# Performance work log

Measured on AMD Instinct MI355X. Metric: run time of the kernel, lower is better.

The kernel has to match this reference:

```python
import jax, jax.numpy as jnp
import numpy as np

D_MODEL = 768
N_HEAD = 12


def setup_inputs() -> dict:
    key = jax.random.key(0)
    ks = jax.random.split(key, 5)
    B, S, D = 2, 4096, D_MODEL
    scale = 0.02
    return {
        "x": jax.random.normal(ks[0], (B, S, D), dtype=jnp.float32),
        "W_in": jax.random.normal(ks[1], (D, 3 * D), dtype=jnp.float32) * scale,
        "b_in": jax.random.normal(ks[2], (3 * D,), dtype=jnp.float32) * scale,
        "W_out": jax.random.normal(ks[3], (D, D), dtype=jnp.float32) * scale,
        "b_out": jax.random.normal(ks[4], (D,), dtype=jnp.float32) * scale,
    }


def reference(x, W_in, b_in, W_out, b_out):
    B, S, D = x.shape
    H = N_HEAD
    d_head = D // H
    qkv = x @ W_in + b_in                      # [B,S,3D]
    q, k, v = jnp.split(qkv, 3, axis=-1)
    # [B,H,S,d]
    q = q.reshape(B, S, H, d_head).transpose(0, 2, 1, 3)
    k = k.reshape(B, S, H, d_head).transpose(0, 2, 1, 3)
    v = v.reshape(B, S, H, d_head).transpose(0, 2, 1, 3)
    att = jnp.einsum("bhqd,bhkd->bhqk", q, k) * (1.0 / jnp.sqrt(jnp.float32(d_head)))
    causal = jnp.tril(jnp.ones((S, S), dtype=bool))
    att = jnp.where(causal[None, None], att, jnp.float32(-jnp.inf))
    att = jax.nn.softmax(att, axis=-1)
    y = jnp.einsum("bhqk,bhkd->bhqd", att, v)  # [B,H,S,d]
    y = y.transpose(0, 2, 1, 3).reshape(B, S, D)
    return y @ W_out + b_out
```

## Files before the change

### kernel.cpp

```cpp
#include <hip/hip_runtime.h>
#include <hip/hip_bf16.h>


#define D_MODEL 768
#define SEQ 4096
#define NB 2
#define NHEAD 12

typedef __attribute__((ext_vector_type(8))) short short8;
typedef __attribute__((ext_vector_type(4))) float floatx4;
typedef __attribute__((ext_vector_type(16))) float floatx16;

#define SM_C 0.18033688011112042f

#if __has_builtin(__builtin_amdgcn_exp2f)
#define EXP2(x) __builtin_amdgcn_exp2f(x)
#else
#define EXP2(x) __expf((x) * 0.6931471805599453f)
#endif

__device__ inline short fb(float f) {
    union { __hip_bfloat16 h; short s; } cv;
    cv.h = __float2bfloat16(f);
    return cv.s;
}
__device__ inline unsigned pk2(float a, float b) {
    float2 f; f.x = a; f.y = b;
    union { __hip_bfloat162 h; unsigned u; } cv;
    cv.h = __float22bfloat162_rn(f);
    return cv.u;
}
__device__ inline void gload16(const void* g, void* l) {
    __builtin_amdgcn_global_load_lds(
        (const __attribute__((address_space(1))) unsigned int*)g,
        (__attribute__((address_space(3))) unsigned int*)l, 16, 0, 0);
}

__global__ __launch_bounds__(256) void convert_bf16(const float* __restrict__ src,
                                                    short* __restrict__ dst, size_t n) {
    size_t i = ((size_t)blockIdx.x * 256 + threadIdx.x) * 8;
    if (i >= n) return;
    float4 f0 = *(const float4*)(src + i);
    float4 f1 = *(const float4*)(src + i + 4);
    uint4 u = {pk2(f0.x, f0.y), pk2(f0.z, f0.w), pk2(f1.x, f1.y), pk2(f1.z, f1.w)};
    *(uint4*)(dst + i) = u;
}

__global__ __launch_bounds__(256) void transpose_bf16(const float* __restrict__ W,
                                                      short* __restrict__ Wt,
                                                      int K, int N) {
    __shared__ short t[32][33];
    const int n0 = blockIdx.x * 32, k0 = blockIdx.y * 32;
    const int tx = threadIdx.x, ty = threadIdx.y;
#pragma unroll
    for (int j = 0; j < 4; ++j)
        t[ty + j * 8][tx] = fb(W[(size_t)(k0 + ty + j * 8) * N + n0 + tx]);
    __syncthreads();
#pragma unroll
    for (int j = 0; j < 4; ++j)
        Wt[(size_t)(n0 + ty + j * 8) * K + k0 + tx] = t[tx][ty + j * 8];
}

__global__ __launch_bounds__(256) void gemm_qkv128(const short* __restrict__ A,
                                                   const short* __restrict__ Bt,
                                                   const float* __restrict__ bias,
                                                   short* __restrict__ qimg,
                                                   short* __restrict__ kimg,
                                                   short* __restrict__ vimg) {
    const int K = D_MODEL;
    __shared__ short As[128][32];
    __shared__ short Bs[128][32];
    const int tid = threadIdx.x, lane = tid & 63, w = tid >> 6;
    const int wr = w >> 1, wc = w & 1;
    const int lo = lane & 15, hi = lane >> 4;
    const int m0 = blockIdx.y * 128, n0 = blockIdx.x * 128;
    const int lr = lane >> 2, lc = (lane & 3) * 8;

    floatx4 acc[4][4] = {};
    const short* Ag = A  + (size_t)(m0 + w * 16 + lr) * K + lc;
    const short* Bg = Bt + (size_t)(n0 + w * 16 + lr) * K + lc;

    for (int k0 = 0; k0 < K; k0 += 32) {
        __syncthreads();
        gload16(Ag + k0,                  &As[w * 16][0]);
        gload16(Ag + k0 + (size_t)64 * K, &As[64 + w * 16][0]);
        gload16(Bg + k0,                  &Bs[w * 16][0]);
        gload16(Bg + k0 + (size_t)64 * K, &Bs[64 + w * 16][0]);
        __syncthreads();
        short8 a[4], bf[4];
#pragma unroll
        for (int m = 0; m < 4; ++m) a[m] = *(const short8*)&As[wr * 64 + m * 16 + lo][hi * 8];
#pragma unroll
        for (int n = 0; n < 4; ++n) bf[n] = *(const short8*)&Bs[wc * 64 + n * 16 + lo][hi * 8];
#pragma unroll
        for (int m = 0; m < 4; ++m)
#pragma unroll
            for (int n = 0; n < 4; ++n)
                acc[m][n] = __builtin_amdgcn_mfma_f32_16x16x32_bf16(a[m], bf[n], acc[m][n], 0, 0, 0);
    }

#pragma unroll
    for (int m = 0; m < 4; ++m)
#pragma unroll
        for (int n = 0; n < 4; ++n) {
            int col  = n0 + wc * 64 + n * 16 + lo;
            int row0 = m0 + wr * 64 + m * 16 + hi * 4;
            float bv = bias[col];
            if (col < D_MODEL) {
                int hq = col >> 6, dh = col & 63;
                int kc = dh >> 4, dl = (dh >> 3) & 1, d7 = dh & 7;
#pragma unroll
                for (int r = 0; r < 4; ++r) {
                    int row = row0 + r;
                    int bb = row >> 12, s = row & 4095;
                    size_t off = (((((size_t)bb * NHEAD + hq) * 64 + (s >> 6)) * 8
                                  + ((s >> 5) & 1) * 4 + kc) * 512)
                               + ((s & 31) + dl * 32) * 8 + d7;
                    qimg[off] = fb((acc[m][n][r] + bv) * SM_C);
                }
            } else if (col < 2 * D_MODEL) {
                int kc2 = col - D_MODEL;
                int hh = kc2 >> 6, dh = kc2 & 63;
                int kc = dh >> 4, dl = (dh >> 3) & 1, d7 = dh & 7;
#pragma unroll
                for (int r = 0; r < 4; ++r) {
                    int row = row0 + r;
                    int bb = row >> 12, s = row & 4095;
                    int kb = s >> 6, kr = s & 63;
                    size_t base = (((size_t)bb * NHEAD + hh) * 64 + kb) * 4096;
                    kimg[base + ((kr >> 5) * 4 + kc) * 512 + ((kr & 31) + dl * 32) * 8 + d7] =
                        fb(acc[m][n][r] + bv);
                }
            } else {
                int vcol = col - 2 * D_MODEL;
                int hh = vcol >> 6, dh = vcol & 63;
                int bb = row0 >> 12, s = row0 & 4095;
                int kb = s >> 6, kr = s & 63;
                size_t base = (((size_t)bb * NHEAD + hh) * 64 + kb) * 4096;
                size_t off = base + ((dh >> 5) * 4 + (kr >> 4)) * 512
                           + ((dh & 31) + ((kr >> 3) & 1) * 32) * 8 + (kr & 7);
                uint2 u = {pk2(acc[m][n][0] + bv, acc[m][n][1] + bv),
                           pk2(acc[m][n][2] + bv, acc[m][n][3] + bv)};
                *(uint2*)&vimg[off] = u;
            }
        }
}

__global__ __launch_bounds__(256) void gemm_out128(const short* __restrict__ A,
                                                   const short* __restrict__ Bt,
                                                   const float* __restrict__ bias,
                                                   float* __restrict__ C) {
    const int K = D_MODEL, N = D_MODEL;
    __shared__ short As[128][32];
    __shared__ short Bs[128][32];
    const int tid = threadIdx.x, lane = tid & 63, w = tid >> 6;
    const int wr = w >> 1, wc = w & 1;
    const int lo = lane & 15, hi = lane >> 4;
    const int m0 = blockIdx.y * 128, n0 = blockIdx.x * 128;
    const int lr = lane >> 2, lc = (lane & 3) * 8;

    floatx4 acc[4][4] = {};
    const short* Ag = A  + (size_t)(m0 + w * 16 + lr) * K + lc;
    const short* Bg = Bt + (size_t)(n0 + w * 16 + lr) * K + lc;

    for (int k0 = 0; k0 < K; k0 += 32) {
        __syncthreads();
        gload16(Ag + k0,                  &As[w * 16][0]);
        gload16(Ag + k0 + (size_t)64 * K, &As[64 + w * 16][0]);
        gload16(Bg + k0,                  &Bs[w * 16][0]);
        gload16(Bg + k0 + (size_t)64 * K, &Bs[64 + w * 16][0]);
        __syncthreads();
        short8 a[4], bf[4];
#pragma unroll
        for (int m = 0; m < 4; ++m) a[m] = *(const short8*)&As[wr * 64 + m * 16 + lo][hi * 8];
#pragma unroll
        for (int n = 0; n < 4; ++n) bf[n] = *(const short8*)&Bs[wc * 64 + n * 16 + lo][hi * 8];
#pragma unroll
        for (int m = 0; m < 4; ++m)
#pragma unroll
            for (int n = 0; n < 4; ++n)
                acc[m][n] = __builtin_amdgcn_mfma_f32_16x16x32_bf16(a[m], bf[n], acc[m][n], 0, 0, 0);
    }

#pragma unroll
    for (int m = 0; m < 4; ++m)
#pragma unroll
        for (int n = 0; n < 4; ++n) {
            int col  = n0 + wc * 64 + n * 16 + lo;
            int row0 = m0 + wr * 64 + m * 16 + hi * 4;
            float bv = bias[col];
#pragma unroll
            for (int r = 0; r < 4; ++r)
                C[(size_t)(row0 + r) * N + col] = acc[m][n][r] + bv;
        }
}

__global__ __launch_bounds__(256, 2) void attn_k(const short* __restrict__ qimg,
                                                 const short* __restrict__ kimg,
                                                 const short* __restrict__ vimg,
                                                 short* __restrict__ y) {
    const int L = blockIdx.x;
    const int xcd = L & 7, slot = L >> 3;
    const int ghead = slot >> 5, ip = slot & 31;
    const int g = ghead * 8 + xcd;
    const int b = g / NHEAD, h = g % NHEAD;
    const int tid = threadIdx.x, lane = tid & 63, w = tid >> 6;
    const int l31 = lane & 31, hh = lane >> 5;

    __shared__ alignas(16) short KL[4][4096];
    __shared__ unsigned LOD[4][2048];
    __shared__ float LS[4][2][2][64];

    const short* kbase = kimg + ((size_t)b * NHEAD + h) * 64 * 4096;
    const short* vbase = vimg + ((size_t)b * NHEAD + h) * 64 * 4096 + lane * 8;
    const short* qtbase = qimg + ((size_t)b * NHEAD + h) * 64 * 4096;
    short* Kbuf = &KL[w][0];

    const int nlo = ip + 1;
    const int npos = ((64 - w) >> 2) + 1;

    if (w >= nlo) {
#pragma unroll
        for (int r = 0; r < 32; ++r) LOD[w][r * 64 + lane] = 0u;
        LS[w][0][0][lane] = 0.0f;
        LS[w][0][1][lane] = 0.0f;
    }

    floatx16 Oa = {}, Ob = {}, Oc = {}, Od = {};
    float ls0 = 0.0f, ls1 = 0.0f;
    short8 qf0[4], qf1[4], vf[8];

    int curtile = (w < nlo) ? ip : (63 - ip);
    {
        const short* qr = qtbase + (size_t)curtile * 4096 + lane * 8;
#pragma unroll
        for (int kc = 0; kc < 4; ++kc) {
            qf0[kc] = *(const short8*)(qr + kc * 512);
            qf1[kc] = *(const short8*)(qr + (4 + kc) * 512);
        }
    }
    {
        int kb0 = (w < nlo) ? w : (w - nlo);
        const short* ks = kbase + (size_t)kb0 * 4096 + lane * 8;
#pragma unroll
        for (int c = 0; c < 8; ++c) gload16(ks + c * 512, Kbuf + c * 512);
        const short* vs = vbase + (size_t)kb0 * 4096;
#pragma unroll
        for (int i = 0; i < 8; ++i) vf[i] = *(const short8*)(vs + i * 512);
    }

    for (int it = 0; it < npos; ++it) {
        const int s = w + 4 * it;
        const int tile = (s < nlo) ? ip : (63 - ip);
        const int kblk = (s < nlo) ? s : (s - nlo);

        if (tile != curtile) {
#pragma unroll
            for (int rp = 0; rp < 8; ++rp) {
                LOD[w][(0 * 8 + rp) * 64 + lane] = pk2(Oa[2 * rp], Oa[2 * rp + 1]);
                LOD[w][(1 * 8 + rp) * 64 + lane] = pk2(Ob[2 * rp], Ob[2 * rp + 1]);
                LOD[w][(2 * 8 + rp) * 64 + lane] = pk2(Oc[2 * rp], Oc[2 * rp + 1]);
                LOD[w][(3 * 8 + rp) * 64 + lane] = pk2(Od[2 * rp], Od[2 * rp + 1]);
            }
            LS[w][0][0][lane] = ls0;
            LS[w][0][1][lane] = ls1;
#pragma unroll
            for (int r = 0; r < 16; ++r) { Oa[r] = 0.0f; Ob[r] = 0.0f; Oc[r] = 0.0f; Od[r] = 0.0f; }
            ls0 = ls1 = 0.0f;
            const short* qr = qtbase + (size_t)tile * 4096 + lane * 8;
#pragma unroll
            for (int kc = 0; kc < 4; ++kc) {
                qf0[kc] = *(const short8*)(qr + kc * 512);
                qf1[kc] = *(const short8*)(qr + (4 + kc) * 512);
            }
            curtile = tile;
        }

        asm volatile("s_waitcnt vmcnt(0)" ::: "memory");
        __builtin_amdgcn_sched_barrier(0);

        floatx16 S00 = {}, S10 = {}, S01 = {}, S11 = {};
        __builtin_amdgcn_s_setprio(1);
#pragma unroll
        for (int kc = 0; kc < 4; ++kc) {
            short8 kf = *(const short8*)&Kbuf[kc * 512 + lane * 8];
            S00 = __builtin_amdgcn_mfma_f32_32x32x16_bf16(kf, qf0[kc], S00, 0, 0, 0);
            S10 = __builtin_amdgcn_mfma_f32_32x32x16_bf16(kf, qf1[kc], S10, 0, 0, 0);
        }
#pragma unroll
        for (int kc = 0; kc < 4; ++kc) {
            short8 kf = *(const short8*)&Kbuf[(4 + kc) * 512 + lane * 8];
            S01 = __builtin_amdgcn_mfma_f32_32x32x16_bf16(kf, qf0[kc], S01, 0, 0, 0);
            S11 = __builtin_amdgcn_mfma_f32_32x32x16_bf16(kf, qf1[kc], S11, 0, 0, 0);
        }
        __builtin_amdgcn_s_setprio(0);
        __builtin_amdgcn_sched_barrier(0);

        if (it + 1 < npos) {
            int sn = s + 4;
            int nk = (sn < nlo) ? sn : (sn - nlo);
            const short* ks = kbase + (size_t)nk * 4096 + lane * 8;
#pragma unroll
            for (int c = 0; c < 8; ++c) gload16(ks + c * 512, Kbuf + c * 512);
        }
        __builtin_amdgcn_sched_barrier(0);

        if (kblk == tile) {
            const int qg0 = tile * 64 + l31, qg1 = qg0 + 32;
#pragma unroll
            for (int kb2 = 0; kb2 < 2; ++kb2) {
                int kb_base = kblk * 64 + kb2 * 32 + 4 * hh;
#pragma unroll
                for (int r = 0; r < 16; ++r) {
                    int kgl = kb_base + (r & 3) + 8 * (r >> 2);
                    if (kb2 == 0) {
                        if (kgl > qg0) S00[r] = -1e30f;
                        if (kgl > qg1) S10[r] = -1e30f;
                    } else {
                        if (kgl > qg0) S01[r] = -1e30f;
                        if (kgl > qg1) S11[r] = -1e30f;
                    }
                }
            }
        }

#pragma unroll
        for (int kb2 = 0; kb2 < 2; ++kb2) {
            {
                floatx16& S = kb2 ? S01 : S00;
                unsigned wA[4], wB[4];
#pragma unroll
                for (int g4 = 0; g4 < 4; ++g4) {
                    float p0 = EXP2(S[4 * g4 + 0]), p1 = EXP2(S[4 * g4 + 1]);
                    float p2 = EXP2(S[4 * g4 + 2]), p3 = EXP2(S[4 * g4 + 3]);
                    ls0 += (p0 + p1) + (p2 + p3);
                    wA[g4] = pk2(p0, p1);
                    wB[g4] = pk2(p2, p3);
                }
#pragma unroll
                for (int c16 = 0; c16 < 2; ++c16) {
                    unsigned xa = wA[2 * c16], ya = wA[2 * c16 + 1];
                    unsigned xb = wB[2 * c16], yb = wB[2 * c16 + 1];
                    asm("v_permlane32_swap_b32 %0, %1" : "+v"(xa), "+v"(ya));
                    asm("v_permlane32_swap_b32 %0, %1" : "+v"(xb), "+v"(yb));
                    union { unsigned u[4]; short8 s8; } pa;
                    pa.u[0] = xa; pa.u[1] = xb; pa.u[2] = ya; pa.u[3] = yb;
                    const int kcg = kb2 * 2 + c16;
                    __builtin_amdgcn_s_setprio(1);
                    Oa = __builtin_amdgcn_mfma_f32_32x32x16_bf16(pa.s8, vf[kcg],     Oa, 0, 0, 0);
                    Ob = __builtin_amdgcn_mfma_f32_32x32x16_bf16(pa.s8, vf[4 + kcg], Ob, 0, 0, 0);
                    __builtin_amdgcn_s_setprio(0);
                }
            }
            {
                floatx16& S = kb2 ? S11 : S10;
                unsigned wA[4], wB[4];
#pragma unroll
                for (int g4 = 0; g4 < 4; ++g4) {
                    float p0 = EXP2(S[4 * g4 + 0]), p1 = EXP2(S[4 * g4 + 1]);
                    float p2 = EXP2(S[4 * g4 + 2]), p3 = EXP2(S[4 * g4 + 3]);
                    ls1 += (p0 + p1) + (p2 + p3);
                    wA[g4] = pk2(p0, p1);
                    wB[g4] = pk2(p2, p3);
                }
#pragma unroll
                for (int c16 = 0; c16 < 2; ++c16) {
                    unsigned xa = wA[2 * c16], ya = wA[2 * c16 + 1];
                    unsigned xb = wB[2 * c16], yb = wB[2 * c16 + 1];
                    asm("v_permlane32_swap_b32 %0, %1" : "+v"(xa), "+v"(ya));
                    asm("v_permlane32_swap_b32 %0, %1" : "+v"(xb), "+v"(yb));
                    union { unsigned u[4]; short8 s8; } pa;
                    pa.u[0] = xa; pa.u[1] = xb; pa.u[2] = ya; pa.u[3] = yb;
                    const int kcg = kb2 * 2 + c16;
                    __builtin_amdgcn_s_setprio(1);
                    Oc = __builtin_amdgcn_mfma_f32_32x32x16_bf16(pa.s8, vf[kcg],     Oc, 0, 0, 0);
                    Od = __builtin_amdgcn_mfma_f32_32x32x16_bf16(pa.s8, vf[4 + kcg], Od, 0, 0, 0);
                    __builtin_amdgcn_s_setprio(0);
                }
            }
        }
        __builtin_amdgcn_sched_barrier(0);

        if (it + 1 < npos) {
            int sn = s + 4;
            int nk = (sn < nlo) ? sn : (sn - nlo);
            const short* vs = vbase + (size_t)nk * 4096;
#pragma unroll
            for (int i = 0; i < 8; ++i) vf[i] = *(const short8*)(vs + i * 512);
        }
        __builtin_amdgcn_sched_barrier(0);
    }

    {
        unsigned* hslot = (unsigned*)&KL[w][0];
#pragma unroll
        for (int rp = 0; rp < 8; ++rp) {
            hslot[(0 * 8 + rp) * 64 + lane] = pk2(Oa[2 * rp], Oa[2 * rp + 1]);
            hslot[(1 * 8 + rp) * 64 + lane] = pk2(Ob[2 * rp], Ob[2 * rp + 1]);
            hslot[(2 * 8 + rp) * 64 + lane] = pk2(Oc[2 * rp], Oc[2 * rp + 1]);
            hslot[(3 * 8 + rp) * 64 + lane] = pk2(Od[2 * rp], Od[2 * rp + 1]);
        }
        LS[w][1][0][lane] = ls0;
        LS[w][1][1][lane] = ls1;
    }
    __syncthreads();

    {
        const int tsel = w >> 1;
        const int fqh = w & 1;
        const int ftile = tsel ? (63 - ip) : ip;

        float lt = 0.0f;
#pragma unroll
        for (int ww = 0; ww < 4; ++ww)
            lt += LS[ww][tsel][fqh][l31] + LS[ww][tsel][fqh][l31 + 32];
        float inv = 1.0f / lt;

#pragma unroll
        for (int dv = 0; dv < 2; ++dv) {
#pragma unroll
            for (int rp = 0; rp < 8; ++rp) {
                float o0 = 0.0f, o1 = 0.0f;
#pragma unroll
                for (int ww = 0; ww < 4; ++ww) {
                    unsigned u = tsel
                        ? ((const unsigned*)&KL[ww][0])[((fqh * 2 + dv) * 8 + rp) * 64 + lane]
                        : LOD[ww][((fqh * 2 + dv) * 8 + rp) * 64 + lane];
                    o0 += __builtin_bit_cast(float, u << 16);
                    o1 += __builtin_bit_cast(float, u & 0xffff0000u);
                }
                int r0 = 2 * rp, r1 = 2 * rp + 1;
                int q0r = (r0 & 3) + 8 * (r0 >> 2) + 4 * hh;
                int q1r = (r1 & 3) + 8 * (r1 >> 2) + 4 * hh;
                float iv0 = __shfl(inv, q0r, 64);
                float iv1 = __shfl(inv, q1r, 64);
                size_t rowb = ((size_t)b * SEQ + ftile * 64 + fqh * 32);
                y[(rowb + q0r) * D_MODEL + h * 64 + dv * 32 + l31] = fb(o0 * iv0);
                y[(rowb + q1r) * D_MODEL + h * 64 + dv * 32 + l31] = fb(o1 * iv1);
            }
        }
    }
}

extern "C" void kernel_launch(void* const* d_in, const int* in_sizes, int n_in,
                              void* d_out, int out_size, void* d_ws, size_t ws_size,
                              hipStream_t stream) {
    (void)in_sizes; (void)n_in; (void)out_size; (void)ws_size;
    const float* x     = (const float*)d_in[0];
    const float* W_in  = (const float*)d_in[1];
    const float* b_in  = (const float*)d_in[2];
    const float* W_out = (const float*)d_in[3];
    const float* b_out = (const float*)d_in[4];
    float* out = (float*)d_out;

    const int M = NB * SEQ;
    char* p = (char*)d_ws;
    short* xbf   = (short*)p; p += (size_t)M * D_MODEL * 2;
    short* wtin  = (short*)p; p += (size_t)3 * D_MODEL * D_MODEL * 2;
    short* wtout = (short*)p; p += (size_t)D_MODEL * D_MODEL * 2;
    short* qimg  = (short*)p; p += (size_t)M * D_MODEL * 2;
    short* kimg  = (short*)p; p += (size_t)NB * NHEAD * 64 * 4096 * 2;
    short* vimg  = (short*)p; p += (size_t)NB * NHEAD * 64 * 4096 * 2;
    short* yw    = (short*)p;

    convert_bf16<<<dim3((unsigned)((size_t)M * D_MODEL / 8 / 256)), 256, 0, stream>>>(
        x, xbf, (size_t)M * D_MODEL);
    transpose_bf16<<<dim3(3 * D_MODEL / 32, D_MODEL / 32), dim3(32, 8), 0, stream>>>(
        W_in, wtin, D_MODEL, 3 * D_MODEL);
    transpose_bf16<<<dim3(D_MODEL / 32, D_MODEL / 32), dim3(32, 8), 0, stream>>>(
        W_out, wtout, D_MODEL, D_MODEL);
    gemm_qkv128<<<dim3(3 * D_MODEL / 128, M / 128), 256, 0, stream>>>(
        xbf, wtin, b_in, qimg, kimg, vimg);
    attn_k<<<dim3(NB * NHEAD * 32), 256, 0, stream>>>(qimg, kimg, vimg, yw);
    gemm_out128<<<dim3(D_MODEL / 128, M / 128), 256, 0, stream>>>(yw, wtout, b_out, out);
}
```

Baseline: 165.2 us.

## Double-buffer V fragments in registers to prefetch next V block earlier

Splits the V register fragments into two ping-pong buffers and unrolls the loop by two, so the next block's V loads are issued at the start of each iteration instead of after the PV MFMAs. The wait before the QK step becomes vmcnt(8), which waits on the earlier K loads while leaving the fresh V loads in flight. The aim is to hide V global-load latency behind QK and softmax compute. In exchange it uses 32 more VGPRs per lane, which may hurt occupancy at the 2-blocks bound or cause spills, and adds an explicit lgkmcnt wait before the K refill.

```diff
diff --git a/kernel.cpp b/kernel.cpp
--- a/kernel.cpp
+++ b/kernel.cpp
@@ -211,7 +211,7 @@
     __shared__ unsigned LOD[4][2048];
     __shared__ float LS[4][2][2][64];
 
-    const short* kbase = kimg + ((size_t)b * NHEAD + h) * 64 * 4096;
+    const short* kbase = kimg + ((size_t)b * NHEAD + h) * 64 * 4096 + lane * 8;
     const short* vbase = vimg + ((size_t)b * NHEAD + h) * 64 * 4096 + lane * 8;
     const short* qtbase = qimg + ((size_t)b * NHEAD + h) * 64 * 4096;
     short* Kbuf = &KL[w][0];
@@ -228,7 +228,7 @@
 
     floatx16 Oa = {}, Ob = {}, Oc = {}, Od = {};
     float ls0 = 0.0f, ls1 = 0.0f;
-    short8 qf0[4], qf1[4], vf[8];
+    short8 qf0[4], qf1[4], vfA[8], vfB[8];
 
     int curtile = (w < nlo) ? ip : (63 - ip);
     {
@@ -241,15 +241,15 @@
     }
     {
         int kb0 = (w < nlo) ? w : (w - nlo);
-        const short* ks = kbase + (size_t)kb0 * 4096 + lane * 8;
+        const short* ks = kbase + (size_t)kb0 * 4096;
 #pragma unroll
         for (int c = 0; c < 8; ++c) gload16(ks + c * 512, Kbuf + c * 512);
         const short* vs = vbase + (size_t)kb0 * 4096;
 #pragma unroll
-        for (int i = 0; i < 8; ++i) vf[i] = *(const short8*)(vs + i * 512);
-    }
-
-    for (int it = 0; it < npos; ++it) {
+        for (int i = 0; i < 8; ++i) vfA[i] = *(const short8*)(vs + i * 512);
+    }
+
+    auto body = [&](int it, short8 (&vcur)[8], short8 (&vnxt)[8]) {
         const int s = w + 4 * it;
         const int tile = (s < nlo) ? ip : (63 - ip);
         const int kblk = (s < nlo) ? s : (s - nlo);
@@ -276,7 +276,16 @@
             curtile = tile;
         }
 
-        asm volatile("s_waitcnt vmcnt(0)" ::: "memory");
+        const bool more = (it + 1 < npos);
+        if (more) {
+            int sn = s + 4;
+            int nk = (sn < nlo) ? sn : (sn - nlo);
+            const short* vs = vbase + (size_t)nk * 4096;
+#pragma unroll
+            for (int i = 0; i < 8; ++i) vnxt[i] = *(const short8*)(vs + i * 512);
+        }
+        if (more) { asm volatile("s_waitcnt vmcnt(8)" ::: "memory"); }
+        else      { asm volatile("s_waitcnt vmcnt(0)" ::: "memory"); }
         __builtin_amdgcn_sched_barrier(0);
 
         floatx16 S00 = {}, S10 = {}, S01 = {}, S11 = {};
@@ -294,12 +303,13 @@
             S11 = __builtin_amdgcn_mfma_f32_32x32x16_bf16(kf, qf1[kc], S11, 0, 0, 0);
         }
         __builtin_amdgcn_s_setprio(0);
+        asm volatile("s_waitcnt lgkmcnt(0)" ::: "memory");
         __builtin_amdgcn_sched_barrier(0);
 
-        if (it + 1 < npos) {
+        if (more) {
             int sn = s + 4;
             int nk = (sn < nlo) ? sn : (sn - nlo);
-            const short* ks = kbase + (size_t)nk * 4096 + lane * 8;
+            const short* ks = kbase + (size_t)nk * 4096;
 #pragma unroll
             for (int c = 0; c < 8; ++c) gload16(ks + c * 512, Kbuf + c * 512);
         }
@@ -347,8 +357,8 @@
                     pa.u[0] = xa; pa.u[1] = xb; pa.u[2] = ya; pa.u[3] = yb;
                     const int kcg = kb2 * 2 + c16;
                     __builtin_amdgcn_s_setprio(1);
-                    Oa = __builtin_amdgcn_mfma_f32_32x32x16_bf16(pa.s8, vf[kcg],     Oa, 0, 0, 0);
-                    Ob = __builtin_amdgcn_mfma_f32_32x32x16_bf16(pa.s8, vf[4 + kcg], Ob, 0, 0, 0);
+                    Oa = __builtin_amdgcn_mfma_f32_32x32x16_bf16(pa.s8, vcur[kcg],     Oa, 0, 0, 0);
+                    Ob = __builtin_amdgcn_mfma_f32_32x32x16_bf16(pa.s8, vcur[4 + kcg], Ob, 0, 0, 0);
                     __builtin_amdgcn_s_setprio(0);
                 }
             }
@@ -373,23 +383,21 @@
                     pa.u[0] = xa; pa.u[1] = xb; pa.u[2] = ya; pa.u[3] = yb;
                     const int kcg = kb2 * 2 + c16;
                     __builtin_amdgcn_s_setprio(1);
-                    Oc = __builtin_amdgcn_mfma_f32_32x32x16_bf16(pa.s8, vf[kcg],     Oc, 0, 0, 0);
-                    Od = __builtin_amdgcn_mfma_f32_32x32x16_bf16(pa.s8, vf[4 + kcg], Od, 0, 0, 0);
+                    Oc = __builtin_amdgcn_mfma_f32_32x32x16_bf16(pa.s8, vcur[kcg],     Oc, 0, 0, 0);
+                    Od = __builtin_amdgcn_mfma_f32_32x32x16_bf16(pa.s8, vcur[4 + kcg], Od, 0, 0, 0);
                     __builtin_amdgcn_s_setprio(0);
                 }
             }
         }
-        __builtin_amdgcn_sched_barrier(0);
-
-        if (it + 1 < npos) {
-            int sn = s + 4;
-            int nk = (sn < nlo) ? sn : (sn - nlo);
-            const short* vs = vbase + (size_t)nk * 4096;
-#pragma unroll
-            for (int i = 0; i < 8; ++i) vf[i] = *(const short8*)(vs + i * 512);
-        }
-        __builtin_amdgcn_sched_barrier(0);
-    }
+    };
+
+    int it = 0;
+    while (it + 2 <= npos) {
+        body(it,     vfA, vfB);
+        body(it + 1, vfB, vfA);
+        it += 2;
+    }
+    if (it < npos) body(it, vfA, vfB);
 
     {
         unsigned* hslot = (unsigned*)&KL[w][0];
```

Result: slower. 229.4 us (+38.9%).
